# Optimization experiments

Measured on AMD Instinct MI355X. Metric: run time of the kernel, lower is better.

Reference implementation:

```python
import jax, jax.numpy as jnp
import numpy as np

B, L, C, H = 4, 2048, 1024, 16
D = C // H            # head_dim = 64
TAU = 4
SCALE = 1.0 / np.sqrt(D) / TAU  # cos_attn=False path


def setup_inputs() -> dict:
    key = jax.random.key(0)
    ks = jax.random.split(key, 7)
    std = 1.0 / np.sqrt(C)
    return {
        "x": jax.random.normal(ks[0], (B, L, C), dtype=jnp.float32),
        "attn_bias": jax.random.normal(ks[1], (1, 1, L, L), dtype=jnp.float32) * 0.02,
        "W_qkv": jax.random.normal(ks[2], (3 * C, C), dtype=jnp.float32) * std,
        "q_bias": jax.random.normal(ks[3], (C,), dtype=jnp.float32) * 0.02,
        "v_bias": jax.random.normal(ks[4], (C,), dtype=jnp.float32) * 0.02,
        "W_proj": jax.random.normal(ks[5], (C, C), dtype=jnp.float32) * std,
        "b_proj": jax.random.normal(ks[6], (C,), dtype=jnp.float32) * 0.02,
    }


def reference(x, attn_bias, W_qkv, q_bias, v_bias, W_proj, b_proj):
    # qkv projection with bias = cat(q_bias, zeros_k, v_bias)
    bias = jnp.concatenate([q_bias, jnp.zeros_like(q_bias), v_bias])
    qkv = x @ W_qkv.T + bias                      # [B, L, 3C]
    qkv = qkv.reshape(B, L, 3, H, D)
    q, k, v = jnp.moveaxis(qkv, 2, 0)             # each [B, L, H, D]
    q = q.transpose(0, 2, 1, 3)                   # [B, H, L, D]
    k = k.transpose(0, 2, 1, 3)
    v = v.transpose(0, 2, 1, 3)
    # slow_attn: (q*scale) @ k^T + bias -> softmax -> @ v
    scores = jnp.einsum("bhqd,bhkd->bhqk", q * SCALE, k) + attn_bias
    attn = jax.nn.softmax(scores, axis=-1)
    oup = jnp.einsum("bhqk,bhkd->bhqd", attn, v)  # [B, H, L, D]
    oup = oup.transpose(0, 2, 1, 3).reshape(B, L, C)
    return oup @ W_proj.T + b_proj
```

## Files before the change

### kernel.cpp

```cpp
#include <hip/hip_runtime.h>
#include <hip/hip_bf16.h>

typedef unsigned short u16;
typedef unsigned int   u32;

using f32x4  = __attribute__((ext_vector_type(4)))  float;
using f32x16 = __attribute__((ext_vector_type(16))) float;
using s16x8  = __attribute__((ext_vector_type(8)))  short;
using b16x8  = __attribute__((ext_vector_type(8)))  __bf16;
using u32x4  = __attribute__((ext_vector_type(4)))  u32;

#define LOG2E 1.44269504088896f
#define QSC   (0.03125f * LOG2E)

__device__ __forceinline__ f32x4 mfma16(s16x8 a, s16x8 b, f32x4 c) {
  return __builtin_amdgcn_mfma_f32_16x16x32_bf16(
      __builtin_bit_cast(b16x8, a), __builtin_bit_cast(b16x8, b), c, 0, 0, 0);
}
__device__ __forceinline__ f32x16 mfma32(s16x8 a, s16x8 b, f32x16 c) {
  return __builtin_amdgcn_mfma_f32_32x32x16_bf16(
      __builtin_bit_cast(b16x8, a), __builtin_bit_cast(b16x8, b), c, 0, 0, 0);
}

__device__ __forceinline__ u16 f2bf(float f) {
  u32 u = __builtin_bit_cast(u32, f);
  u = (u + 0x7FFFu + ((u >> 16) & 1u)) >> 16;
  return (u16)u;
}
__device__ __forceinline__ float exp2_hw(float x) {
  float r;
  asm("v_exp_f32 %0, %1" : "=v"(r) : "v"(x));
  return r;
}
__device__ __forceinline__ u32 cvtpk(float a, float b) {
  u32 r;
  asm("v_cvt_pk_bf16_f32 %0, %1, %2" : "=v"(r) : "v"(a), "v"(b));
  return r;
}

__device__ __forceinline__ void gload16(const void* g, void* l) {
  __builtin_amdgcn_global_load_lds(
      (const __attribute__((address_space(1))) u32*)g,
      (__attribute__((address_space(3))) u32*)l, 16, 0, 0);
}

__global__ void cvt(const float* __restrict__ in, u16* __restrict__ out, int n4) {
  int i = blockIdx.x * blockDim.x + threadIdx.x;
  int stride = gridDim.x * blockDim.x;
  for (; i < n4; i += stride) {
    float4 v = ((const float4*)in)[i];
    ushort4 o;
    o.x = f2bf(v.x); o.y = f2bf(v.y); o.z = f2bf(v.z); o.w = f2bf(v.w);
    ((ushort4*)out)[i] = o;
  }
}

__global__ void bias_rearrange(const float* __restrict__ ab, u16* __restrict__ out) {
  const int idx  = blockIdx.x * 256 + threadIdx.x;
  const int lane = idx & 63;
  const int vo   = ((idx >> 6) & 3) * 8;
  const int kt   = (idx >> 8) & 31;
  const int qi   = (idx >> 13) & 1;
  const int w    = (idx >> 14) & 3;
  const int qt   = (idx >> 16) & 7;
  const int hi   = lane >> 5;
  const int q    = qt * 256 + w * 64 + qi * 32 + (lane & 31);
  const int kb   = vo >> 4;
  const int so   = (vo & 8) << 1;
  const int kbase = kt * 64 + kb * 32 + so + 4 * hi;
  const float* src = ab + (long)q * 2048 + kbase;
  const float4 a = *(const float4*)(src);
  const float4 b = *(const float4*)(src + 8);
  u16 o[8];
  o[0] = f2bf(a.x * LOG2E); o[1] = f2bf(a.y * LOG2E);
  o[2] = f2bf(a.z * LOG2E); o[3] = f2bf(a.w * LOG2E);
  o[4] = f2bf(b.x * LOG2E); o[5] = f2bf(b.y * LOG2E);
  o[6] = f2bf(b.z * LOG2E); o[7] = f2bf(b.w * LOG2E);
  *(s16x8*)(out + (long)idx * 8) = *(s16x8*)o;
}

template<int EPI>
__global__ __launch_bounds__(256)
void gemm_bt(const u16* __restrict__ A, const u16* __restrict__ Bm,
             int M, int N, int K,
             const float* __restrict__ bias0, const float* __restrict__ bias1,
             u16* __restrict__ oq, u16* __restrict__ ok, u16* __restrict__ ov,
             float* __restrict__ outf)
{
  __shared__ u16 As[2][128 * 32];
  __shared__ u16 Bs[2][128 * 32];

  const int tid  = threadIdx.x;
  const int w    = tid >> 6;
  const int lane = tid & 63;
  const int lr   = lane & 15;
  const int lg   = lane >> 4;
  const int wr   = w >> 1, wc = w & 1;

  const int bm = blockIdx.y, bn = blockIdx.x;

  f32x4 acc[4][4];
#pragma unroll
  for (int i = 0; i < 4; ++i)
#pragma unroll
    for (int j = 0; j < 4; ++j) acc[i][j] = (f32x4){0.f, 0.f, 0.f, 0.f};

  const int rowA = bm * 128 + (tid >> 2);
  const int rowB = bn * 128 + (tid >> 2);
  const int colk = (tid & 3) * 8;

  const u16* ga0 = A  + (long)rowA * K + colk;
  const u16* gb0 = Bm + (long)rowB * K + colk;

  gload16(ga0,          &As[0][w * 512]);
  gload16(ga0 + 64 * K, &As[0][2048 + w * 512]);
  gload16(gb0,          &Bs[0][w * 512]);
  gload16(gb0 + 64 * K, &Bs[0][2048 + w * 512]);
  asm volatile("s_waitcnt vmcnt(0)" ::: "memory");
  __syncthreads();

  const int NT = K >> 5;
  for (int t = 0; t < NT; ++t) {
    const int cur = t & 1;
    if (t + 1 < NT) {
      const u16* ga = ga0 + (t + 1) * 32;
      const u16* gb = gb0 + (t + 1) * 32;
      gload16(ga,          &As[cur ^ 1][w * 512]);
      gload16(ga + 64 * K, &As[cur ^ 1][2048 + w * 512]);
      gload16(gb,          &Bs[cur ^ 1][w * 512]);
      gload16(gb + 64 * K, &Bs[cur ^ 1][2048 + w * 512]);
    }

    s16x8 af[4], bfr[4];
#pragma unroll
    for (int mi = 0; mi < 4; ++mi)
      af[mi] = *(const s16x8*)(&As[cur][(wr * 64 + mi * 16 + lr) * 32 + lg * 8]);
#pragma unroll
    for (int ni = 0; ni < 4; ++ni)
      bfr[ni] = *(const s16x8*)(&Bs[cur][(wc * 64 + ni * 16 + lr) * 32 + lg * 8]);
#pragma unroll
    for (int mi = 0; mi < 4; ++mi)
#pragma unroll
      for (int ni = 0; ni < 4; ++ni)
        acc[mi][ni] = mfma16(af[mi], bfr[ni], acc[mi][ni]);

    asm volatile("s_waitcnt vmcnt(0)" ::: "memory");
    __syncthreads();
  }

  const int gm0 = bm * 128 + wr * 64;
  const int gn0 = bn * 128 + wc * 64;

#pragma unroll
  for (int mi = 0; mi < 4; ++mi) {
#pragma unroll
    for (int ni = 0; ni < 4; ++ni) {
      const int col  = gn0 + ni * 16 + lr;
      const int row0 = gm0 + mi * 16 + lg * 4;
      if (EPI == 0) {
        const int which = col >> 10;
        const int cj    = col & 1023;
        const float badd = (which == 0) ? bias0[cj] : (which == 2 ? bias1[cj] : 0.f);
        const int h = cj >> 6, d = cj & 63;
#pragma unroll
        for (int r = 0; r < 4; ++r) {
          const int rowg = row0 + r;
          const int b = rowg >> 11, l = rowg & 2047;
          const int bh = b * 16 + h;
          float val = acc[mi][ni][r] + badd;
          if (which == 0) val *= QSC;
          const u16 o = f2bf(val);
          if (which == 0)      oq[(bh * 2048 + l) * 64 + d] = o;
          else if (which == 1) ok[(bh * 2048 + l) * 64 + d] = o;
          else {
            const int lp = (l & ~12) | ((l & 4) << 1) | ((l & 8) >> 1);
            ov[(bh * 64 + d) * 2048 + lp] = o;
          }
        }
      } else {
        const float badd = bias0[col];
#pragma unroll
        for (int r = 0; r < 4; ++r)
          outf[(long)(row0 + r) * N + col] = acc[mi][ni][r] + badd;
      }
    }
  }
}

__global__ __launch_bounds__(256)
void flash_attn(const u16* __restrict__ qbuf, const u16* __restrict__ kbuf,
                const u16* __restrict__ vtbuf, const u16* __restrict__ biasr,
                u16* __restrict__ oup)
{
  __shared__ u32 Os[4][32][33];

  const int tid  = threadIdx.x;
  const int w    = tid >> 6;
  const int lane = tid & 63;
  const int lq   = lane & 31;
  const int hi   = lane >> 5;

  const int bid = blockIdx.x;
  const int wg  = (bid & 7) * 64 + (bid >> 3);
  const int bh  = wg >> 3, qt = wg & 7;
  const long base = (long)bh * (2048 * 64);

  s16x8 qf[2][4];
#pragma unroll
  for (int qi = 0; qi < 2; ++qi) {
    const int qrow = qt * 256 + w * 64 + qi * 32 + lq;
    const u16* qp = qbuf + base + qrow * 64 + 8 * hi;
#pragma unroll
    for (int s = 0; s < 4; ++s) qf[qi][s] = *(const s16x8*)(qp + 16 * s);
  }

  f32x16 oacc[2][2];
  float lacc[2][8];
#pragma unroll
  for (int qi = 0; qi < 2; ++qi) {
#pragma unroll
    for (int r = 0; r < 16; ++r) { oacc[qi][0][r] = 0.f; oacc[qi][1][r] = 0.f; }
#pragma unroll
    for (int r = 0; r < 8; ++r) lacc[qi][r] = 0.f;
  }

  const u16* bslice = biasr + (long)((qt * 4 + w) * 2) * 65536 + lane * 8;

  for (int kt = 0; kt < 32; ++kt) {
    const u16* kp = kbuf + base + (kt * 64 + lq) * 64 + 8 * hi;
    s16x8 kf0[4], kf1[4];
#pragma unroll
    for (int s = 0; s < 4; ++s) {
      kf0[s] = *(const s16x8*)(kp + 16 * s);
      kf1[s] = *(const s16x8*)(kp + 2048 + 16 * s);
    }

    const u16* vp = vtbuf + base + lq * 2048 + kt * 64 + 8 * hi;
    s16x8 vf0[4], vf1[4];
#pragma unroll
    for (int ks = 0; ks < 4; ++ks) {
      vf0[ks] = *(const s16x8*)(vp + 16 * ks);
      vf1[ks] = *(const s16x8*)(vp + 32 * 2048 + 16 * ks);
    }

    u32x4 bb[2][4];
#pragma unroll
    for (int qi = 0; qi < 2; ++qi)
#pragma unroll
      for (int k = 0; k < 4; ++k)
        bb[qi][k] = *(const u32x4*)(bslice + (long)qi * 65536 + kt * 2048 + k * 512);

#pragma unroll
    for (int qi = 0; qi < 2; ++qi) {
      f32x16 sa0, sa1;
#pragma unroll
      for (int jw = 0; jw < 8; ++jw) {
        const u32 w0 = bb[qi][jw >> 2][jw & 3];
        const u32 w1 = bb[qi][2 + (jw >> 2)][jw & 3];
        sa0[2 * jw]     = __builtin_bit_cast(float, w0 << 16);
        sa0[2 * jw + 1] = __builtin_bit_cast(float, w0 & 0xFFFF0000u);
        sa1[2 * jw]     = __builtin_bit_cast(float, w1 << 16);
        sa1[2 * jw + 1] = __builtin_bit_cast(float, w1 & 0xFFFF0000u);
      }

#pragma unroll
      for (int s = 0; s < 4; ++s) sa0 = mfma32(kf0[s], qf[qi][s], sa0);
#pragma unroll
      for (int s = 0; s < 4; ++s) sa1 = mfma32(kf1[s], qf[qi][s], sa1);

#pragma unroll
      for (int r = 0; r < 16; ++r) {
        sa0[r] = exp2_hw(sa0[r]);
        sa1[r] = exp2_hw(sa1[r]);
      }
#pragma unroll
      for (int r = 0; r < 8; ++r)
        lacc[qi][r] += (sa0[r] + sa0[r + 8]) + (sa1[r] + sa1[r + 8]);

      s16x8 pf[4];
#pragma unroll
      for (int ks = 0; ks < 4; ++ks) {
        const f32x16 ps = (ks & 2) ? sa1 : sa0;
        const int o = (ks & 1) * 8;
        u32x4 tt;
        tt[0] = cvtpk(ps[o + 0], ps[o + 1]);
        tt[1] = cvtpk(ps[o + 2], ps[o + 3]);
        tt[2] = cvtpk(ps[o + 4], ps[o + 5]);
        tt[3] = cvtpk(ps[o + 6], ps[o + 7]);
        pf[ks] = __builtin_bit_cast(s16x8, tt);
      }

#pragma unroll
      for (int ks = 0; ks < 4; ++ks) {
        oacc[qi][0] = mfma32(vf0[ks], pf[ks], oacc[qi][0]);
        oacc[qi][1] = mfma32(vf1[ks], pf[ks], oacc[qi][1]);
      }
    }
  }

  const int b = bh >> 4, h = bh & 15;
#pragma unroll
  for (int qi = 0; qi < 2; ++qi) {
    float l = ((lacc[qi][0] + lacc[qi][1]) + (lacc[qi][2] + lacc[qi][3]))
            + ((lacc[qi][4] + lacc[qi][5]) + (lacc[qi][6] + lacc[qi][7]));
    l += __shfl_xor(l, 32, 64);
    const float inv = 1.f / l;
#pragma unroll
    for (int i = 0; i < 8; ++i) {
      const int idx = (i & 1) + 2 * hi + 4 * (i >> 1);
      Os[w][lq][idx]      = cvtpk(oacc[qi][0][2 * i] * inv, oacc[qi][0][2 * i + 1] * inv);
      Os[w][lq][idx + 16] = cvtpk(oacc[qi][1][2 * i] * inv, oacc[qi][1][2 * i + 1] * inv);
    }
    __syncthreads();
#pragma unroll
    for (int it = 0; it < 4; ++it) {
      const int q = it * 8 + (lane >> 3);
      const int c = (lane & 7) * 4;
      u32x4 v;
#pragma unroll
      for (int j = 0; j < 4; ++j) v[j] = Os[w][q][c + j];
      const long row = (long)(b * 2048 + qt * 256 + w * 64 + qi * 32 + q);
      *(u32x4*)(oup + row * 1024 + h * 64 + (lane & 7) * 8) = v;
    }
    __syncthreads();
  }
}

extern "C" void kernel_launch(void* const* d_in, const int* in_sizes, int n_in,
                              void* d_out, int out_size, void* d_ws, size_t ws_size,
                              hipStream_t stream) {
  const float* x     = (const float*)d_in[0];
  const float* ab    = (const float*)d_in[1];
  const float* wqkv  = (const float*)d_in[2];
  const float* qbias = (const float*)d_in[3];
  const float* vbias = (const float*)d_in[4];
  const float* wproj = (const float*)d_in[5];
  const float* bproj = (const float*)d_in[6];
  float* out = (float*)d_out;

  char* ws = (char*)d_ws;
  if (ws_size < 83886080u) return;
  u16* xb     = (u16*)(ws);
  u16* wqkvb  = (u16*)(ws + 16777216);
  u16* wprojb = (u16*)(ws + 23068672);
  u16* biasr  = (u16*)(ws + 25165824);
  u16* qbuf   = (u16*)(ws + 33554432);
  u16* kbuf   = (u16*)(ws + 50331648);
  u16* vtbuf  = (u16*)(ws + 67108864);

  cvt<<<dim3(2048), dim3(256), 0, stream>>>(x, xb, 8388608 / 4);
  cvt<<<dim3(512),  dim3(256), 0, stream>>>(wqkv, wqkvb, 3145728 / 4);
  cvt<<<dim3(256),  dim3(256), 0, stream>>>(wproj, wprojb, 1048576 / 4);
  bias_rearrange<<<dim3(2048), dim3(256), 0, stream>>>(ab, biasr);

  gemm_bt<0><<<dim3(24, 64), dim3(256), 0, stream>>>(
      xb, wqkvb, 8192, 3072, 1024, qbias, vbias, qbuf, kbuf, vtbuf, nullptr);

  flash_attn<<<dim3(512), dim3(256), 0, stream>>>(qbuf, kbuf, vtbuf, biasr, xb);

  gemm_bt<1><<<dim3(8, 64), dim3(256), 0, stream>>>(
      xb, wprojb, 8192, 1024, 1024, bproj, nullptr, nullptr, nullptr, nullptr, out);
}
```

Baseline: 273.9 us.

## Double-buffer K/V register fragments and raise wave priority around MFMAs

```diff
diff --git a/kernel.cpp b/kernel.cpp
--- a/kernel.cpp
+++ b/kernel.cpp
@@ -225,78 +225,91 @@
   }
 
   const u16* bslice = biasr + (long)((qt * 4 + w) * 2) * 65536 + lane * 8;
-
-  for (int kt = 0; kt < 32; ++kt) {
-    const u16* kp = kbuf + base + (kt * 64 + lq) * 64 + 8 * hi;
-    s16x8 kf0[4], kf1[4];
-#pragma unroll
-    for (int s = 0; s < 4; ++s) {
-      kf0[s] = *(const s16x8*)(kp + 16 * s);
-      kf1[s] = *(const s16x8*)(kp + 2048 + 16 * s);
-    }
-
-    const u16* vp = vtbuf + base + lq * 2048 + kt * 64 + 8 * hi;
-    s16x8 vf0[4], vf1[4];
-#pragma unroll
-    for (int ks = 0; ks < 4; ++ks) {
-      vf0[ks] = *(const s16x8*)(vp + 16 * ks);
-      vf1[ks] = *(const s16x8*)(vp + 32 * 2048 + 16 * ks);
-    }
-
-    u32x4 bb[2][4];
-#pragma unroll
-    for (int qi = 0; qi < 2; ++qi)
-#pragma unroll
-      for (int k = 0; k < 4; ++k)
-        bb[qi][k] = *(const u32x4*)(bslice + (long)qi * 65536 + kt * 2048 + k * 512);
-
-#pragma unroll
-    for (int qi = 0; qi < 2; ++qi) {
-      f32x16 sa0, sa1;
-#pragma unroll
-      for (int jw = 0; jw < 8; ++jw) {
-        const u32 w0 = bb[qi][jw >> 2][jw & 3];
-        const u32 w1 = bb[qi][2 + (jw >> 2)][jw & 3];
-        sa0[2 * jw]     = __builtin_bit_cast(float, w0 << 16);
-        sa0[2 * jw + 1] = __builtin_bit_cast(float, w0 & 0xFFFF0000u);
-        sa1[2 * jw]     = __builtin_bit_cast(float, w1 << 16);
-        sa1[2 * jw + 1] = __builtin_bit_cast(float, w1 & 0xFFFF0000u);
-      }
-
-#pragma unroll
-      for (int s = 0; s < 4; ++s) sa0 = mfma32(kf0[s], qf[qi][s], sa0);
-#pragma unroll
-      for (int s = 0; s < 4; ++s) sa1 = mfma32(kf1[s], qf[qi][s], sa1);
-
-#pragma unroll
-      for (int r = 0; r < 16; ++r) {
-        sa0[r] = exp2_hw(sa0[r]);
-        sa1[r] = exp2_hw(sa1[r]);
-      }
-#pragma unroll
-      for (int r = 0; r < 8; ++r)
-        lacc[qi][r] += (sa0[r] + sa0[r + 8]) + (sa1[r] + sa1[r + 8]);
-
-      s16x8 pf[4];
-#pragma unroll
-      for (int ks = 0; ks < 4; ++ks) {
-        const f32x16 ps = (ks & 2) ? sa1 : sa0;
-        const int o = (ks & 1) * 8;
-        u32x4 tt;
-        tt[0] = cvtpk(ps[o + 0], ps[o + 1]);
-        tt[1] = cvtpk(ps[o + 2], ps[o + 3]);
-        tt[2] = cvtpk(ps[o + 4], ps[o + 5]);
-        tt[3] = cvtpk(ps[o + 6], ps[o + 7]);
-        pf[ks] = __builtin_bit_cast(s16x8, tt);
-      }
-
-#pragma unroll
-      for (int ks = 0; ks < 4; ++ks) {
-        oacc[qi][0] = mfma32(vf0[ks], pf[ks], oacc[qi][0]);
-        oacc[qi][1] = mfma32(vf1[ks], pf[ks], oacc[qi][1]);
-      }
-    }
-  }
+  const u16* kbase_p = kbuf  + base + lq * 64 + 8 * hi;
+  const u16* vbase_p = vtbuf + base + lq * 2048 + 8 * hi;
+
+  s16x8 kf0A[4], kf1A[4], vf0A[4], vf1A[4];
+  s16x8 kf0B[4], kf1B[4], vf0B[4], vf1B[4];
+
+#define LOADF(K0, K1, V0, V1, KT)                                   \
+  {                                                                 \
+    const int kt_ = (KT) & 31;                                      \
+    const u16* kp_ = kbase_p + kt_ * 4096;                          \
+    const u16* vp_ = vbase_p + kt_ * 64;                            \
+    _Pragma("unroll")                                               \
+    for (int s = 0; s < 4; ++s) {                                   \
+      K0[s] = *(const s16x8*)(kp_ + 16 * s);                        \
+      K1[s] = *(const s16x8*)(kp_ + 2048 + 16 * s);                 \
+      V0[s] = *(const s16x8*)(vp_ + 16 * s);                        \
+      V1[s] = *(const s16x8*)(vp_ + 32 * 2048 + 16 * s);            \
+    }                                                               \
+  }
+
+#define COMPUTE(K0, K1, V0, V1, KT)                                              \
+  {                                                                              \
+    u32x4 bb[2][4];                                                              \
+    _Pragma("unroll")                                                            \
+    for (int qi = 0; qi < 2; ++qi)                                               \
+      _Pragma("unroll")                                                          \
+      for (int k = 0; k < 4; ++k)                                                \
+        bb[qi][k] = *(const u32x4*)(bslice + (long)qi * 65536 + (KT) * 2048 + k * 512); \
+    _Pragma("unroll")                                                            \
+    for (int qi = 0; qi < 2; ++qi) {                                             \
+      f32x16 sa0, sa1;                                                           \
+      _Pragma("unroll")                                                          \
+      for (int jw = 0; jw < 8; ++jw) {                                           \
+        const u32 w0 = bb[qi][jw >> 2][jw & 3];                                  \
+        const u32 w1 = bb[qi][2 + (jw >> 2)][jw & 3];                            \
+        sa0[2 * jw]     = __builtin_bit_cast(float, w0 << 16);                   \
+        sa0[2 * jw + 1] = __builtin_bit_cast(float, w0 & 0xFFFF0000u);           \
+        sa1[2 * jw]     = __builtin_bit_cast(float, w1 << 16);                   \
+        sa1[2 * jw + 1] = __builtin_bit_cast(float, w1 & 0xFFFF0000u);           \
+      }                                                                          \
+      __builtin_amdgcn_s_setprio(1);                                             \
+      _Pragma("unroll")                                                          \
+      for (int s = 0; s < 4; ++s) sa0 = mfma32(K0[s], qf[qi][s], sa0);           \
+      _Pragma("unroll")                                                          \
+      for (int s = 0; s < 4; ++s) sa1 = mfma32(K1[s], qf[qi][s], sa1);           \
+      __builtin_amdgcn_s_setprio(0);                                             \
+      _Pragma("unroll")                                                          \
+      for (int r = 0; r < 16; ++r) {                                             \
+        sa0[r] = exp2_hw(sa0[r]);                                                \
+        sa1[r] = exp2_hw(sa1[r]);                                                \
+      }                                                                          \
+      _Pragma("unroll")                                                          \
+      for (int r = 0; r < 8; ++r)                                                \
+        lacc[qi][r] += (sa0[r] + sa0[r + 8]) + (sa1[r] + sa1[r + 8]);            \
+      s16x8 pf[4];                                                               \
+      _Pragma("unroll")                                                          \
+      for (int ks = 0; ks < 4; ++ks) {                                           \
+        const f32x16 ps = (ks & 2) ? sa1 : sa0;                                  \
+        const int o = (ks & 1) * 8;                                              \
+        u32x4 tt;                                                                \
+        tt[0] = cvtpk(ps[o + 0], ps[o + 1]);                                     \
+        tt[1] = cvtpk(ps[o + 2], ps[o + 3]);                                     \
+        tt[2] = cvtpk(ps[o + 4], ps[o + 5]);                                     \
+        tt[3] = cvtpk(ps[o + 6], ps[o + 7]);                                     \
+        pf[ks] = __builtin_bit_cast(s16x8, tt);                                  \
+      }                                                                          \
+      __builtin_amdgcn_s_setprio(1);                                             \
+      _Pragma("unroll")                                                          \
+      for (int ks = 0; ks < 4; ++ks) {                                           \
+        oacc[qi][0] = mfma32(V0[ks], pf[ks], oacc[qi][0]);                       \
+        oacc[qi][1] = mfma32(V1[ks], pf[ks], oacc[qi][1]);                       \
+      }                                                                          \
+      __builtin_amdgcn_s_setprio(0);                                             \
+    }                                                                            \
+  }
+
+  LOADF(kf0A, kf1A, vf0A, vf1A, 0);
+  for (int kt = 0; kt < 32; kt += 2) {
+    LOADF(kf0B, kf1B, vf0B, vf1B, kt + 1);
+    COMPUTE(kf0A, kf1A, vf0A, vf1A, kt);
+    LOADF(kf0A, kf1A, vf0A, vf1A, kt + 2);
+    COMPUTE(kf0B, kf1B, vf0B, vf1B, kt + 1);
+  }
+#undef LOADF
+#undef COMPUTE
 
   const int b = bh >> 4, h = bh & 15;
 #pragma unroll
```

New measurement: 280.3 us. 1.02x slower.

## Stage K/V tiles through double-buffered LDS shared across waves in flash attention

Applied to the files above, without the earlier changes.

```diff
diff --git a/kernel.cpp b/kernel.cpp
--- a/kernel.cpp
+++ b/kernel.cpp
@@ -192,6 +192,8 @@
                 const u16* __restrict__ vtbuf, const u16* __restrict__ biasr,
                 u16* __restrict__ oup)
 {
+  __shared__ u16 Ks[2][64 * 72];
+  __shared__ u16 Vs[2][64 * 72];
   __shared__ u32 Os[4][32][33];
 
   const int tid  = threadIdx.x;
@@ -226,21 +228,50 @@
 
   const u16* bslice = biasr + (long)((qt * 4 + w) * 2) * 65536 + lane * 8;
 
+  const int sr  = tid >> 3;
+  const int scc = tid & 7;
+  const u16* kg = kbuf  + base + sr * 64   + scc * 8;
+  const u16* vg = vtbuf + base + sr * 2048 + scc * 8;
+  const int wo0 = sr * 72 + scc * 8;
+  const int wo1 = (32 + sr) * 72 + scc * 8;
+
+  {
+    const s16x8 a0 = *(const s16x8*)(kg);
+    const s16x8 a1 = *(const s16x8*)(kg + 2048);
+    const s16x8 b0 = *(const s16x8*)(vg);
+    const s16x8 b1 = *(const s16x8*)(vg + 65536);
+    *(s16x8*)(&Ks[0][wo0]) = a0;  *(s16x8*)(&Ks[0][wo1]) = a1;
+    *(s16x8*)(&Vs[0][wo0]) = b0;  *(s16x8*)(&Vs[0][wo1]) = b1;
+  }
+  __syncthreads();
+
   for (int kt = 0; kt < 32; ++kt) {
-    const u16* kp = kbuf + base + (kt * 64 + lq) * 64 + 8 * hi;
-    s16x8 kf0[4], kf1[4];
-#pragma unroll
-    for (int s = 0; s < 4; ++s) {
-      kf0[s] = *(const s16x8*)(kp + 16 * s);
-      kf1[s] = *(const s16x8*)(kp + 2048 + 16 * s);
-    }
-
-    const u16* vp = vtbuf + base + lq * 2048 + kt * 64 + 8 * hi;
-    s16x8 vf0[4], vf1[4];
-#pragma unroll
-    for (int ks = 0; ks < 4; ++ks) {
-      vf0[ks] = *(const s16x8*)(vp + 16 * ks);
-      vf1[ks] = *(const s16x8*)(vp + 32 * 2048 + 16 * ks);
+    const int cur = kt & 1;
+
+    s16x8 nk0, nk1, nv0, nv1;
+    if (kt < 31) {
+      const u16* kn = kg + (kt + 1) * 4096;
+      const u16* vn = vg + (kt + 1) * 64;
+      nk0 = *(const s16x8*)(kn);
+      nk1 = *(const s16x8*)(kn + 2048);
+      nv0 = *(const s16x8*)(vn);
+      nv1 = *(const s16x8*)(vn + 65536);
+    }
+
+    s16x8 kf0[4], kf1[4], vf0[4], vf1[4];
+    {
+      const u16* kb0 = &Ks[cur][lq * 72];
+      const u16* kb1 = &Ks[cur][(32 + lq) * 72];
+      const u16* vb0 = &Vs[cur][lq * 72];
+      const u16* vb1 = &Vs[cur][(32 + lq) * 72];
+#pragma unroll
+      for (int s = 0; s < 4; ++s) {
+        const int off = (2 * s + hi) * 8;
+        kf0[s] = *(const s16x8*)(kb0 + off);
+        kf1[s] = *(const s16x8*)(kb1 + off);
+        vf0[s] = *(const s16x8*)(vb0 + off);
+        vf1[s] = *(const s16x8*)(vb1 + off);
+      }
     }
 
     u32x4 bb[2][4];
@@ -296,6 +327,14 @@
         oacc[qi][1] = mfma32(vf1[ks], pf[ks], oacc[qi][1]);
       }
     }
+
+    if (kt < 31) {
+      *(s16x8*)(&Ks[cur ^ 1][wo0]) = nk0;
+      *(s16x8*)(&Ks[cur ^ 1][wo1]) = nk1;
+      *(s16x8*)(&Vs[cur ^ 1][wo0]) = nv0;
+      *(s16x8*)(&Vs[cur ^ 1][wo1]) = nv1;
+    }
+    __syncthreads();
   }
 
   const int b = bh >> 4, h = bh & 15;
```

Result: faster. 253.6 us (-7.4%).
